# Optimization experiments

Measured on AMD Instinct MI355X. Metric: run time of the kernel, lower is better.

## Reference

```python
import jax, jax.numpy as jnp
import numpy as np

QTZ_BETA = 0.25


def setup_inputs() -> dict:
    key = jax.random.key(0)
    k1, k2 = jax.random.split(key)
    z = jax.random.normal(k1, (65536, 1, 256), dtype=jnp.float32)
    codebook = jax.random.normal(k2, (4096, 256), dtype=jnp.float32)
    return {"z": z, "codebook": codebook}


def reference(z, codebook):
    """Hard VQ quantization: nearest-codebook lookup with straight-through
    estimator plus codebook commitment loss. Returns (z_q, codebook_loss,
    min_embed_ids)."""
    D = codebook.shape[-1]
    z_f = z.reshape(-1, D)  # [N, D]
    # Pairwise squared L2 distances via expansion: ||z||^2 - 2 z c^T + ||c||^2
    # (argmin is invariant to the monotone transform vs. torch.cdist's sqrt)
    d2 = (
        jnp.sum(z_f * z_f, axis=1, keepdims=True)  # [N, 1]
        - 2.0 * (z_f @ codebook.T)                 # [N, K]
        + jnp.sum(codebook * codebook, axis=1)     # [K]
    )
    min_embed_ids = jnp.argmin(d2, axis=1)  # [N]
    # one_hot @ codebook is exactly a gather of codebook rows
    z_q = jnp.take(codebook, min_embed_ids, axis=0).reshape(z.shape)
    # Straight-through estimator
    z_q = z + jax.lax.stop_gradient(z_q - z)
    # Codebook loss (uses the STE z_q, matching the torch code)
    codebook_loss = (
        jnp.mean((jax.lax.stop_gradient(z_q) - z) ** 2)
        + jnp.mean((z_q - jax.lax.stop_gradient(z)) ** 2) * QTZ_BETA
    )
    return (z_q, codebook_loss, min_embed_ids)
```

## Files before the change

kernel.cpp:

```cpp
#include <hip/hip_runtime.h>
#include <stdint.h>

typedef _Float16 f16;
typedef _Float16 f16x4 __attribute__((ext_vector_type(4)));
typedef _Float16 f16x8 __attribute__((ext_vector_type(8)));
typedef float f32x4 __attribute__((ext_vector_type(4)));
typedef unsigned long long u64;

#define D_DIM 256
#define K_CB 4096
#define N_ROWS 65536
#define BM 128
#define BN 128
#define N_TILES 32
#define LOSS_OFF 16777216
#define IDS_OFF 16777217
#define MAX_FIX 4096

#define WS_CHI 0
#define WS_CN 2097152
#define WS_CNT 2113536
#define WS_ROWS 2113600
#define WS_SLOTS 2129984

#define LDS_BYTES 81920

#define GL_LDS(g, s_) __builtin_amdgcn_global_load_lds( \
    (const __attribute__((address_space(1))) void*)(g), \
    (__attribute__((address_space(3))) void*)(s_), 16, 0, 0)

static __device__ __forceinline__ uint32_t f2u(float x) { union { float f; uint32_t u; } c; c.f = x; return c.u; }
static __device__ __forceinline__ float u2f(uint32_t x) { union { float f; uint32_t u; } c; c.u = x; return c.f; }
static __device__ __forceinline__ uint32_t umin_(uint32_t a, uint32_t b) { return a < b ? a : b; }
static __device__ __forceinline__ uint32_t umax_(uint32_t a, uint32_t b) { return a > b ? a : b; }
static __device__ __forceinline__ u64 d2u(double x) { union { double d; u64 u; } c; c.d = x; return c.u; }

static __device__ __forceinline__ uint32_t med3u(uint32_t a, uint32_t b, uint32_t c) {
    uint32_t d;
    asm("v_med3_u32 %0, %1, %2, %3" : "=v"(d) : "v"(a), "v"(b), "v"(c));
    return d;
}
static __device__ __forceinline__ uint32_t min3u(uint32_t a, uint32_t b, uint32_t c) {
    uint32_t d;
    asm("v_min3_u32 %0, %1, %2, %3" : "=v"(d) : "v"(a), "v"(b), "v"(c));
    return d;
}

#define INS3(s_, kk_) do { \
    const uint32_t kkv_ = (kk_); \
    const uint32_t n1_ = umin_(k1[s_], kkv_); \
    const uint32_t n2_ = med3u(kkv_, k1[s_], k2[s_]); \
    const uint32_t n3_ = med3u(kkv_, k2[s_], k3[s_]); \
    k1[s_] = n1_; k2[s_] = n2_; k3[s_] = n3_; \
} while (0)

__global__ __launch_bounds__(256) void k_prep_cb(const float* __restrict__ cb,
                                                 f16* __restrict__ chi,
                                                 float* __restrict__ cn,
                                                 uint32_t* __restrict__ cnt,
                                                 u64* __restrict__ slots,
                                                 float* __restrict__ loss_slot) {
    const int tid = threadIdx.x;
    const int w = tid >> 6, l = tid & 63;
    const int row = blockIdx.x * 4 + w;
    const float4 v = ((const float4*)cb)[row * 64 + l];
    f16x4 h4;
    h4[0] = (f16)v.x; h4[1] = (f16)v.y; h4[2] = (f16)v.z; h4[3] = (f16)v.w;
    float ss = v.x * v.x + v.y * v.y + v.z * v.z + v.w * v.w;
#pragma unroll
    for (int m = 32; m >= 1; m >>= 1) ss += __shfl_xor(ss, m);
    ((f16x4*)chi)[row * 64 + l] = h4;
    if (l == 0) cn[row] = ss;
    if (tid < 4) slots[blockIdx.x * 4 + tid] = 0xFFFFFFFFFFFFFFFFull;
    if (blockIdx.x == 0 && tid == 0) { *cnt = 0; *loss_slot = 0.0f; }
}

#define TILE_BODY(ACC, PREV, TILE) do { \
    const int tile_ = (TILE); \
    _Pragma("unroll") for (int j = 0; j < 4; ++j) cnCur[j] = cnNext[j]; \
    _Pragma("unroll") for (int j = 0; j < 4; ++j) { \
        const float base_ = cnCur[j] + 64.0f; \
        _Pragma("unroll") for (int i = 0; i < 4; ++i) \
            ACC[i][j] = (f32x4){base_, base_, base_, base_}; \
    } \
    const int prevColb_ = (tile_ - 1) * BN + wn * 64 + l15; \
    _Pragma("unroll") for (int kc = 0; kc < 8; ++kc) { \
        const int step_ = tile_ * 8 + kc; \
        asm volatile("s_waitcnt vmcnt(0)" ::: "memory"); \
        __builtin_amdgcn_s_barrier(); \
        __builtin_amdgcn_sched_barrier(0); \
        if (step_ + 1 < N_TILES * 8) { \
            const int nt_ = (step_ + 1) >> 3, nk_ = (step_ + 1) & 7; \
            const f16* gh_ = chi + nt_ * (BN * D_DIM) + nk_ * 32 + offE; \
            char* bb_ = smem + 65536 + ((kc + 1) & 1) * 8192 + w * 1024; \
            GL_LDS(gh_, bb_); \
            GL_LDS(gh_ + 16384, bb_ + 4096); \
        } \
        if (kc == 0) { \
            const int tn_ = (tile_ + 1 < N_TILES) ? tile_ + 1 : tile_; \
            _Pragma("unroll") for (int j = 0; j < 4; ++j) \
                cnNext[j] = cn[tn_ * BN + wn * 64 + j * 16 + l15]; \
        } \
        const char* bbase_ = smem + 65536 + (kc & 1) * 8192; \
        f16x8 ah[4], bh[4]; \
        _Pragma("unroll") for (int i = 0; i < 4; ++i) \
            ah[i] = *(const f16x8*)(smem + ab + kc * 8192 + i * 1024); \
        _Pragma("unroll") for (int j = 0; j < 4; ++j) \
            bh[j] = *(const f16x8*)(bbase_ + bcon[j]); \
        {  \
            const int pi_ = kc >> 1; \
            _Pragma("unroll") for (int jj = 0; jj < 2; ++jj) { \
                const int pj_ = (kc & 1) * 2 + jj; \
                const uint32_t col_ = (uint32_t)(prevColb_ + pj_ * 16); \
                _Pragma("unroll") for (int rr = 0; rr < 4; ++rr) { \
                    const uint32_t kk_ = (f2u(PREV[pi_][pj_][rr]) & 0xFFFFF000u) | col_; \
                    INS3(pi_ * 4 + rr, kk_); \
                } \
            } \
        } \
        _Pragma("unroll") for (int i = 0; i < 4; ++i) \
            _Pragma("unroll") for (int j = 0; j < 4; ++j) \
                ACC[i][j] = __builtin_amdgcn_mfma_f32_16x16x32_f16(ah[i], bh[j], ACC[i][j], 0, 0, 0); \
    } \
} while (0)

__global__ __launch_bounds__(256, 2) void k_main(const float* __restrict__ z,
                                                 const float* __restrict__ cb,
                                                 const f16* __restrict__ chi,
                                                 const float* __restrict__ cn,
                                                 uint32_t* __restrict__ cnt,
                                                 uint32_t* __restrict__ rows,
                                                 float* __restrict__ out) {
    extern __shared__ char smem[];
    const int tid = threadIdx.x;
    const int w = tid >> 6, l = tid & 63;
    const int wm = w >> 1, wn = w & 1;
    const int l15 = l & 15, qh = l >> 4;
    const int blk = blockIdx.x;
    const float* ztile = z + (size_t)blk * (BM * D_DIM);

    const int e0 = tid >> 2;
    const int q0 = (tid & 3) ^ ((e0 >> 1) & 3);
    const int offE = e0 * 256 + q0 * 8;

    {
        const f16* gh = chi + offE;
        char* bb = smem + 65536 + w * 1024;
        GL_LDS(gh, bb);
        GL_LDS(gh + 16384, bb + 4096);
    }

#pragma unroll 4
    for (int p = 0; p < 32; ++p) {
        const int r = p * 4 + w;
        const float4 v = ((const float4*)ztile)[r * 64 + l];
        f16x4 h4;
        h4[0] = (f16)(v.x * -2.0f); h4[1] = (f16)(v.y * -2.0f);
        h4[2] = (f16)(v.z * -2.0f); h4[3] = (f16)(v.w * -2.0f);
        const int kcw = l >> 3, q = (l >> 1) & 3, half = l & 1;
        const int addr = kcw * 8192 + r * 64 + (((q ^ ((r >> 1) & 3))) << 4) + half * 8;
        *(f16x4*)(smem + addr) = h4;
    }

    float cnNext[4];
#pragma unroll
    for (int j = 0; j < 4; ++j) cnNext[j] = cn[wn * 64 + j * 16 + l15];

    const int ab = wm * 4096 + l15 * 64 + ((qh ^ ((l15 >> 1) & 3)) << 4);

    int bcon[4];
#pragma unroll
    for (int j = 0; j < 4; ++j) {
        const int e = wn * 64 + j * 16 + l15;
        bcon[j] = e * 64 + ((qh ^ ((e >> 1) & 3)) << 4);
    }

    uint32_t k1[16], k2[16], k3[16];
#pragma unroll
    for (int s = 0; s < 16; ++s) { k1[s] = 0xFFFFFFFFu; k2[s] = 0xFFFFFFFFu; k3[s] = 0xFFFFFFFFu; }

    f32x4 accA[4][4], accB[4][4];
    {
        const float iv = __builtin_inff();
#pragma unroll
        for (int i = 0; i < 4; ++i)
#pragma unroll
            for (int j = 0; j < 4; ++j) accB[i][j] = (f32x4){iv, iv, iv, iv};
    }
    float cnCur[4];

    __syncthreads();

    for (int tp = 0; tp < N_TILES; tp += 2) {
        TILE_BODY(accA, accB, tp);
        TILE_BODY(accB, accA, tp + 1);
    }
    {
        const int colb = (N_TILES - 1) * BN + wn * 64 + l15;
#pragma unroll
        for (int j = 0; j < 4; ++j) {
            const uint32_t col = (uint32_t)(colb + j * 16);
#pragma unroll
            for (int i = 0; i < 4; ++i)
#pragma unroll
                for (int rr = 0; rr < 4; ++rr) {
                    const uint32_t kk = (f2u(accB[i][j][rr]) & 0xFFFFF000u) | col;
                    INS3(i * 4 + rr, kk);
                }
        }
    }

#pragma unroll
    for (int s = 0; s < 16; ++s) {
        uint32_t a1 = k1[s], a2 = k2[s], a3 = k3[s];
#pragma unroll
        for (int m = 1; m <= 8; m <<= 1) {
            const uint32_t b1 = (uint32_t)__shfl_xor((int)a1, m);
            const uint32_t b2 = (uint32_t)__shfl_xor((int)a2, m);
            const uint32_t b3 = (uint32_t)__shfl_xor((int)a3, m);
            const uint32_t r1 = umin_(a1, b1);
            const uint32_t r2 = min3u(a2, b2, umax_(a1, b1));
            const uint32_t r3 = min3u(umax_(a1, b2), umax_(a2, b1), umin_(a3, b3));
            a1 = r1; a2 = r2; a3 = r3;
        }
        k1[s] = a1; k2[s] = a2; k3[s] = a3;
    }
    __syncthreads();
    uint32_t* mk = (uint32_t*)(smem + 65536);
    double* lossW = (double*)(smem + 65536 + 1536);
    if (wn == 0 && l15 == 0) {
#pragma unroll
        for (int s = 0; s < 16; ++s) {
            const int row = wm * 64 + (s >> 2) * 16 + qh * 4 + (s & 3);
            mk[row] = k1[s]; mk[128 + row] = k2[s]; mk[256 + row] = k3[s];
        }
    }
    __syncthreads();
    if (wn == 1 && l15 == 0) {
#pragma unroll
        for (int s = 0; s < 16; ++s) {
            const int row = wm * 64 + (s >> 2) * 16 + qh * 4 + (s & 3);
            const uint32_t b1 = mk[row], b2 = mk[128 + row], b3 = mk[256 + row];
            mk[row] = umin_(k1[s], b1);
            mk[128 + row] = min3u(k2[s], b2, umax_(k1[s], b1));
            mk[256 + row] = min3u(umax_(k1[s], b2), umax_(k2[s], b1), umin_(k3[s], b3));
        }
    }
    __syncthreads();

    double lossAcc = 0.0;
    for (int it = 0; it < 32; ++it) {
        const int row = it * 4 + w;
        const uint32_t K1 = mk[row], K2 = mk[128 + row], K3 = mk[256 + row];
        const int col1 = (int)(K1 & 4095u), col2 = (int)(K2 & 4095u);
        const float4 c1 = ((const float4*)cb)[col1 * 64 + l];
        const float4 c2 = ((const float4*)cb)[col2 * 64 + l];
        const float4 z4 = ((const float4*)ztile)[row * 64 + l];
        double e1, e2;
        {
            const double dx1 = (double)c1.x - z4.x, dy1 = (double)c1.y - z4.y;
            const double dz1 = (double)c1.z - z4.z, dw1 = (double)c1.w - z4.w;
            e1 = dx1 * dx1 + dy1 * dy1 + dz1 * dz1 + dw1 * dw1;
            const double dx2 = (double)c2.x - z4.x, dy2 = (double)c2.y - z4.y;
            const double dz2 = (double)c2.z - z4.z, dw2 = (double)c2.w - z4.w;
            e2 = dx2 * dx2 + dy2 * dy2 + dz2 * dz2 + dw2 * dw2;
        }
        float zn2 = z4.x * z4.x + z4.y * z4.y + z4.z * z4.z + z4.w * z4.w;
#pragma unroll
        for (int m = 32; m >= 1; m >>= 1) {
            e1 += __shfl_xor(e1, m);
            e2 += __shfl_xor(e2, m);
            zn2 += __shfl_xor(zn2, m);
        }
        const bool take1 = (e1 < e2) || (e1 == e2 && col1 <= col2);
        const float4 cw = take1 ? c1 : c2;
        ((float4*)out)[(blk * BM + row) * 64 + l] = cw;
        if (l == 0) {
            const int colw = take1 ? col1 : col2;
            const double ew = take1 ? e1 : e2;
            out[IDS_OFF + blk * BM + row] = (float)colw;
            lossAcc += ew;
            const float d3 = u2f(K3 & 0xFFFFF000u) + zn2 - 64.0f;
            const float eps = 0.006f * sqrtf(zn2) + 0.01f;
            if (!((float)ew < d3 - eps)) {
                const uint32_t e = atomicAdd(cnt, 1u);
                if (e < MAX_FIX) rows[e] = (uint32_t)(blk * BM + row);
            }
        }
    }
    if (l == 0) lossW[w] = lossAcc;
    __syncthreads();
    if (tid == 0) {
        const double tot = (lossW[0] + lossW[1] + lossW[2] + lossW[3]) * (1.25 / 16777216.0);
        atomicAdd(out + LOSS_OFF, (float)tot);
    }
}

__global__ __launch_bounds__(256) void k_fix_scan(const float* __restrict__ z,
                                                  const float* __restrict__ cb,
                                                  const uint32_t* __restrict__ cnt,
                                                  const uint32_t* __restrict__ rows,
                                                  u64* __restrict__ slots) {
    __shared__ float zrow[256];
    __shared__ u64 wmin[4];
    const int tid = threadIdx.x;
    const int w = tid >> 6, l = tid & 63;
    const int chunk = blockIdx.x & 15;
    uint32_t n = *cnt; if (n > MAX_FIX) n = MAX_FIX;
    for (uint32_t e = blockIdx.x >> 4; e < n; e += 64) {
        const int row = (int)rows[e];
        __syncthreads();
        if (tid < 64) ((float4*)zrow)[tid] = ((const float4*)z)[row * 64 + tid];
        __syncthreads();
        const int c = chunk * 256 + tid;
        const float4* crow = (const float4*)(cb + (size_t)c * 256);
        double s = 0.0;
        for (int q = 0; q < 64; ++q) {
            const float4 cv = crow[q];
            const float4 zv = ((const float4*)zrow)[q];
            const double dx = (double)cv.x - zv.x, dy = (double)cv.y - zv.y;
            const double dz = (double)cv.z - zv.z, dw = (double)cv.w - zv.w;
            s += dx * dx + dy * dy + dz * dz + dw * dw;
        }
        u64 key = (d2u(s) & 0xFFFFFFFFFFFFF000ull) | (u64)c;
#pragma unroll
        for (int m = 32; m >= 1; m >>= 1) {
            const u64 o = __shfl_xor(key, m);
            if (o < key) key = o;
        }
        if (l == 0) wmin[w] = key;
        __syncthreads();
        if (tid == 0) {
            u64 k = wmin[0];
            if (wmin[1] < k) k = wmin[1];
            if (wmin[2] < k) k = wmin[2];
            if (wmin[3] < k) k = wmin[3];
            atomicMin(&slots[e], k);
        }
    }
}

__global__ __launch_bounds__(256) void k_fix_patch(const float* __restrict__ z,
                                                   const float* __restrict__ cb,
                                                   const uint32_t* __restrict__ cnt,
                                                   const uint32_t* __restrict__ rows,
                                                   const u64* __restrict__ slots,
                                                   float* __restrict__ out) {
    const int tid = threadIdx.x;
    uint32_t n = *cnt; if (n > MAX_FIX) n = MAX_FIX;
    for (uint32_t e = blockIdx.x; e < n; e += 256) {
        const int row = (int)rows[e];
        const int newc = (int)(slots[e] & 4095ull);
        const int oldc = (int)out[IDS_OFF + row];
        if (newc == oldc) continue;
        double dOld = 0.0, dNew = 0.0;
        if (tid < 64) {
            const float4 zv = ((const float4*)z)[row * 64 + tid];
            const float4 co = ((const float4*)cb)[oldc * 64 + tid];
            const float4 cn4 = ((const float4*)cb)[newc * 64 + tid];
            const double ax = (double)co.x - zv.x, ay = (double)co.y - zv.y;
            const double az = (double)co.z - zv.z, aw = (double)co.w - zv.w;
            dOld = ax * ax + ay * ay + az * az + aw * aw;
            const double bx = (double)cn4.x - zv.x, by = (double)cn4.y - zv.y;
            const double bz = (double)cn4.z - zv.z, bw = (double)cn4.w - zv.w;
            dNew = bx * bx + by * by + bz * bz + bw * bw;
            ((float4*)out)[row * 64 + tid] = cn4;
        }
#pragma unroll
        for (int m = 32; m >= 1; m >>= 1) {
            dOld += __shfl_xor(dOld, m);
            dNew += __shfl_xor(dNew, m);
        }
        if (tid == 0) {
            out[IDS_OFF + row] = (float)newc;
            atomicAdd(out + LOSS_OFF, (float)((dNew - dOld) * (1.25 / 16777216.0)));
        }
    }
}

extern "C" void kernel_launch(void* const* d_in, const int* in_sizes, int n_in,
                              void* d_out, int out_size, void* d_ws, size_t ws_size,
                              hipStream_t stream) {
    (void)in_sizes; (void)n_in; (void)out_size; (void)ws_size;
    const float* z = (const float*)d_in[0];
    const float* cb = (const float*)d_in[1];
    float* out = (float*)d_out;
    char* ws = (char*)d_ws;
    f16* chi = (f16*)(ws + WS_CHI);
    float* cn = (float*)(ws + WS_CN);
    uint32_t* cnt = (uint32_t*)(ws + WS_CNT);
    uint32_t* rows = (uint32_t*)(ws + WS_ROWS);
    u64* slots = (u64*)(ws + WS_SLOTS);

    hipFuncSetAttribute((const void*)k_main,
                        hipFuncAttributeMaxDynamicSharedMemorySize, LDS_BYTES);

    k_prep_cb<<<K_CB / 4, 256, 0, stream>>>(cb, chi, cn, cnt, slots, out + LOSS_OFF);
    k_main<<<N_ROWS / BM, 256, LDS_BYTES, stream>>>(z, cb, chi, cn, cnt, rows, out);
    k_fix_scan<<<1024, 256, 0, stream>>>(z, cb, cnt, rows, slots);
    k_fix_patch<<<256, 256, 0, stream>>>(z, cb, cnt, rows, slots, out);
}
```

Before: 292.2 us.

## Deepen B-tile prefetch to 4 stages, keep A fragments in registers, stage norms in LDS

The codebook B-tile ring grows from a 2-stage to a 4-stage buffer with prefetch three steps ahead, and the wait drops from vmcnt(0) to vmcnt(2) so global loads overlap more of the MFMA work. The z-tile A fragments are loaded into registers once instead of being re-read from LDS every k-step. B fragments are double-buffered in registers, and codebook norms are copied to LDS up front. In exchange, LDS rises to 112 KB and register use grows, so launch bounds drop to one block per CU, lowering occupancy.

```diff
diff --git a/kernel.cpp b/kernel.cpp
--- a/kernel.cpp
+++ b/kernel.cpp
@@ -13,6 +13,7 @@
 #define BM 128
 #define BN 128
 #define N_TILES 32
+#define N_STEPS 256
 #define LOSS_OFF 16777216
 #define IDS_OFF 16777217
 #define MAX_FIX 4096
@@ -23,7 +24,10 @@
 #define WS_ROWS 2113600
 #define WS_SLOTS 2129984
 
-#define LDS_BYTES 81920
+#define A_BASE 0
+#define B_BASE 65536
+#define CN_BASE 98304
+#define LDS_BYTES 114688
 
 #define GL_LDS(g, s_) __builtin_amdgcn_global_load_lds( \
     (const __attribute__((address_space(1))) void*)(g), \
@@ -75,38 +79,112 @@
     if (blockIdx.x == 0 && tid == 0) { *cnt = 0; *loss_slot = 0.0f; }
 }
 
+__global__ __launch_bounds__(256, 1) void k_main(const float* __restrict__ z,
+                                                 const float* __restrict__ cb,
+                                                 const f16* __restrict__ chi,
+                                                 const float* __restrict__ cn,
+                                                 uint32_t* __restrict__ cnt,
+                                                 uint32_t* __restrict__ rows,
+                                                 float* __restrict__ out) {
+    extern __shared__ char smem[];
+    const int tid = threadIdx.x;
+    const int w = tid >> 6, l = tid & 63;
+    const int wm = w >> 1, wn = w & 1;
+    const int l15 = l & 15, qh = l >> 4;
+    const int blk = blockIdx.x;
+    const float* ztile = z + (size_t)blk * (BM * D_DIM);
+
+    const int e0 = tid >> 2;
+    const int q0 = (tid & 3) ^ ((e0 >> 1) & 3);
+    const int offE = e0 * 256 + q0 * 8;
+
+#pragma unroll
+    for (int s = 0; s < 3; ++s) {
+        const f16* gh = chi + s * 32 + offE;
+        char* bb = smem + B_BASE + s * 8192 + w * 1024;
+        GL_LDS(gh, bb);
+        GL_LDS(gh + 16384, bb + 4096);
+    }
+
+#pragma unroll
+    for (int c4 = 0; c4 < 4; ++c4)
+        ((float4*)(smem + CN_BASE))[c4 * 256 + tid] = ((const float4*)cn)[c4 * 256 + tid];
+
+#pragma unroll 4
+    for (int p = 0; p < 32; ++p) {
+        const int r = p * 4 + w;
+        const float4 v = ((const float4*)ztile)[r * 64 + l];
+        f16x4 h4;
+        h4[0] = (f16)(v.x * -2.0f); h4[1] = (f16)(v.y * -2.0f);
+        h4[2] = (f16)(v.z * -2.0f); h4[3] = (f16)(v.w * -2.0f);
+        const int kcw = l >> 3, q = (l >> 1) & 3, half = l & 1;
+        const int addr = A_BASE + kcw * 8192 + r * 64 + (((q ^ ((r >> 1) & 3))) << 4) + half * 8;
+        *(f16x4*)(smem + addr) = h4;
+    }
+
+    const int ab = A_BASE + wm * 4096 + l15 * 64 + ((qh ^ ((l15 >> 1) & 3)) << 4);
+    int bcon[4];
+#pragma unroll
+    for (int j = 0; j < 4; ++j) {
+        const int e = wn * 64 + j * 16 + l15;
+        bcon[j] = B_BASE + e * 64 + ((qh ^ ((e >> 1) & 3)) << 4);
+    }
+    const int cnA = CN_BASE + wn * 256 + l15 * 4;
+
+    uint32_t k1[16], k2[16], k3[16];
+#pragma unroll
+    for (int s = 0; s < 16; ++s) { k1[s] = 0xFFFFFFFFu; k2[s] = 0xFFFFFFFFu; k3[s] = 0xFFFFFFFFu; }
+
+    __syncthreads();
+
+    f16x8 aF[4][8];
+#pragma unroll
+    for (int i = 0; i < 4; ++i)
+#pragma unroll
+        for (int kcc = 0; kcc < 8; ++kcc)
+            aF[i][kcc] = *(const f16x8*)(smem + ab + kcc * 8192 + i * 1024);
+
+    f16x8 bh[2][4];
+#pragma unroll
+    for (int j = 0; j < 4; ++j) bh[0][j] = *(const f16x8*)(smem + bcon[j]);
+
+    float cnNext[4];
+#pragma unroll
+    for (int j = 0; j < 4; ++j) cnNext[j] = *(const float*)(smem + cnA + j * 64);
+
+    f32x4 accA[4][4], accB[4][4];
+    {
+        const float iv = __builtin_inff();
+#pragma unroll
+        for (int i = 0; i < 4; ++i)
+#pragma unroll
+            for (int j = 0; j < 4; ++j) accB[i][j] = (f32x4){iv, iv, iv, iv};
+    }
+
 #define TILE_BODY(ACC, PREV, TILE) do { \
     const int tile_ = (TILE); \
-    _Pragma("unroll") for (int j = 0; j < 4; ++j) cnCur[j] = cnNext[j]; \
     _Pragma("unroll") for (int j = 0; j < 4; ++j) { \
-        const float base_ = cnCur[j] + 64.0f; \
+        const float base_ = cnNext[j] + 64.0f; \
         _Pragma("unroll") for (int i = 0; i < 4; ++i) \
             ACC[i][j] = (f32x4){base_, base_, base_, base_}; \
     } \
     const int prevColb_ = (tile_ - 1) * BN + wn * 64 + l15; \
     _Pragma("unroll") for (int kc = 0; kc < 8; ++kc) { \
-        const int step_ = tile_ * 8 + kc; \
-        asm volatile("s_waitcnt vmcnt(0)" ::: "memory"); \
+        asm volatile("s_waitcnt vmcnt(2)" ::: "memory"); \
         __builtin_amdgcn_s_barrier(); \
         __builtin_amdgcn_sched_barrier(0); \
-        if (step_ + 1 < N_TILES * 8) { \
-            const int nt_ = (step_ + 1) >> 3, nk_ = (step_ + 1) & 7; \
-            const f16* gh_ = chi + nt_ * (BN * D_DIM) + nk_ * 32 + offE; \
-            char* bb_ = smem + 65536 + ((kc + 1) & 1) * 8192 + w * 1024; \
-            GL_LDS(gh_, bb_); \
-            GL_LDS(gh_ + 16384, bb_ + 4096); \
-        } \
+        { int s3 = tile_ * 8 + kc + 3; if (s3 > N_STEPS - 1) s3 = N_STEPS - 1; \
+          const f16* gh_ = chi + (s3 >> 3) * (BN * D_DIM) + (s3 & 7) * 32 + offE; \
+          char* bb_ = smem + B_BASE + (((kc) + 3) & 3) * 8192 + w * 1024; \
+          GL_LDS(gh_, bb_); \
+          GL_LDS(gh_ + 16384, bb_ + 4096); } \
         if (kc == 0) { \
             const int tn_ = (tile_ + 1 < N_TILES) ? tile_ + 1 : tile_; \
             _Pragma("unroll") for (int j = 0; j < 4; ++j) \
-                cnNext[j] = cn[tn_ * BN + wn * 64 + j * 16 + l15]; \
+                cnNext[j] = *(const float*)(smem + cnA + tn_ * 512 + j * 64); \
         } \
-        const char* bbase_ = smem + 65536 + (kc & 1) * 8192; \
-        f16x8 ah[4], bh[4]; \
-        _Pragma("unroll") for (int i = 0; i < 4; ++i) \
-            ah[i] = *(const f16x8*)(smem + ab + kc * 8192 + i * 1024); \
         _Pragma("unroll") for (int j = 0; j < 4; ++j) \
-            bh[j] = *(const f16x8*)(bbase_ + bcon[j]); \
+            bh[(kc + 1) & 1][j] = *(const f16x8*)(smem + bcon[j] + (((kc) + 1) & 3) * 8192); \
         {  \
             const int pi_ = kc >> 1; \
             _Pragma("unroll") for (int jj = 0; jj < 2; ++jj) { \
@@ -120,81 +198,17 @@
         } \
         _Pragma("unroll") for (int i = 0; i < 4; ++i) \
             _Pragma("unroll") for (int j = 0; j < 4; ++j) \
-                ACC[i][j] = __builtin_amdgcn_mfma_f32_16x16x32_f16(ah[i], bh[j], ACC[i][j], 0, 0, 0); \
+                ACC[i][j] = __builtin_amdgcn_mfma_f32_16x16x32_f16(aF[i][kc], bh[kc & 1][j], ACC[i][j], 0, 0, 0); \
     } \
 } while (0)
-
-__global__ __launch_bounds__(256, 2) void k_main(const float* __restrict__ z,
-                                                 const float* __restrict__ cb,
-                                                 const f16* __restrict__ chi,
-                                                 const float* __restrict__ cn,
-                                                 uint32_t* __restrict__ cnt,
-                                                 uint32_t* __restrict__ rows,
-                                                 float* __restrict__ out) {
-    extern __shared__ char smem[];
-    const int tid = threadIdx.x;
-    const int w = tid >> 6, l = tid & 63;
-    const int wm = w >> 1, wn = w & 1;
-    const int l15 = l & 15, qh = l >> 4;
-    const int blk = blockIdx.x;
-    const float* ztile = z + (size_t)blk * (BM * D_DIM);
-
-    const int e0 = tid >> 2;
-    const int q0 = (tid & 3) ^ ((e0 >> 1) & 3);
-    const int offE = e0 * 256 + q0 * 8;
-
-    {
-        const f16* gh = chi + offE;
-        char* bb = smem + 65536 + w * 1024;
-        GL_LDS(gh, bb);
-        GL_LDS(gh + 16384, bb + 4096);
-    }
-
-#pragma unroll 4
-    for (int p = 0; p < 32; ++p) {
-        const int r = p * 4 + w;
-        const float4 v = ((const float4*)ztile)[r * 64 + l];
-        f16x4 h4;
-        h4[0] = (f16)(v.x * -2.0f); h4[1] = (f16)(v.y * -2.0f);
-        h4[2] = (f16)(v.z * -2.0f); h4[3] = (f16)(v.w * -2.0f);
-        const int kcw = l >> 3, q = (l >> 1) & 3, half = l & 1;
-        const int addr = kcw * 8192 + r * 64 + (((q ^ ((r >> 1) & 3))) << 4) + half * 8;
-        *(f16x4*)(smem + addr) = h4;
-    }
-
-    float cnNext[4];
-#pragma unroll
-    for (int j = 0; j < 4; ++j) cnNext[j] = cn[wn * 64 + j * 16 + l15];
-
-    const int ab = wm * 4096 + l15 * 64 + ((qh ^ ((l15 >> 1) & 3)) << 4);
-
-    int bcon[4];
-#pragma unroll
-    for (int j = 0; j < 4; ++j) {
-        const int e = wn * 64 + j * 16 + l15;
-        bcon[j] = e * 64 + ((qh ^ ((e >> 1) & 3)) << 4);
-    }
-
-    uint32_t k1[16], k2[16], k3[16];
-#pragma unroll
-    for (int s = 0; s < 16; ++s) { k1[s] = 0xFFFFFFFFu; k2[s] = 0xFFFFFFFFu; k3[s] = 0xFFFFFFFFu; }
-
-    f32x4 accA[4][4], accB[4][4];
-    {
-        const float iv = __builtin_inff();
-#pragma unroll
-        for (int i = 0; i < 4; ++i)
-#pragma unroll
-            for (int j = 0; j < 4; ++j) accB[i][j] = (f32x4){iv, iv, iv, iv};
-    }
-    float cnCur[4];
-
-    __syncthreads();
 
     for (int tp = 0; tp < N_TILES; tp += 2) {
         TILE_BODY(accA, accB, tp);
         TILE_BODY(accB, accA, tp + 1);
     }
+#undef TILE_BODY
+    asm volatile("s_waitcnt vmcnt(0)" ::: "memory");
+
     {
         const int colb = (N_TILES - 1) * BN + wn * 64 + l15;
 #pragma unroll
@@ -226,8 +240,8 @@
         k1[s] = a1; k2[s] = a2; k3[s] = a3;
     }
     __syncthreads();
-    uint32_t* mk = (uint32_t*)(smem + 65536);
-    double* lossW = (double*)(smem + 65536 + 1536);
+    uint32_t* mk = (uint32_t*)(smem + CN_BASE);
+    double* lossW = (double*)(smem + CN_BASE + 1536);
     if (wn == 0 && l15 == 0) {
 #pragma unroll
         for (int s = 0; s < 16; ++s) {
```

Result: slower. 352.2 us (+20.5%).
